# Optimization experiments

Hardware: AMD Instinct MI355X
Metric: run time of the kernel (lower is better)

Reference implementation:

```python
import jax, jax.numpy as jnp
import numpy as np

B, H, N, D = 4, 16, 2048, 128  # batch, num_head, maxlen, head_dim (qkdim == vdim)
EPS = 1e-6


def _act(x):
    # '1+elu' kernel feature map
    return jax.nn.elu(x) + 1.0


def _simple_rms_norm(x):
    # SimpleRMSNorm over the last dim: x / sqrt(mean(x^2) + eps), no learned scale
    ms = jnp.mean(jnp.square(x), axis=-1, keepdims=True)
    return x * jax.lax.rsqrt(ms + EPS)


def setup_inputs() -> dict:
    key = jax.random.key(0)
    kq, kk, kv, km = jax.random.split(key, 4)
    Q = jax.random.normal(kq, (B, H, N, D), dtype=jnp.float32)
    K = jax.random.normal(kk, (B, H, N, D), dtype=jnp.float32)
    V = jax.random.normal(kv, (B, H, N, D), dtype=jnp.float32)
    mask = jax.random.uniform(km, (B, N), dtype=jnp.float32)
    return {"Q": Q, "K": K, "V": V, "mask": mask}


def reference(Q, K, V, mask):
    m = mask[:, None, :, None]           # (B, 1, N, 1)
    Qf = _act(Q)                          # (B, H, N, D)
    Kf = _act(K) * m                      # masked feature-mapped keys
    Vf = V * m                            # masked values
    # non-causal linear attention: KV = sum_n K_n (x) V_n ; out = Q @ KV
    KV = jnp.einsum('bhnd,bhne->bhde', Kf, Vf)    # (B, H, D, D)
    out = jnp.einsum('bhde,bhnd->bhne', KV, Qf)   # (B, H, N, D)
    return _simple_rms_norm(out)
```

## Files before the change

### kernel.cpp

```cpp
#include <hip/hip_runtime.h>
#include <hip/hip_bf16.h>

#define NBH 64
#define NSEQ 2048
#define DD 128
#define EPS 1e-6f
#define NCH 16
#define CHROWS 128

typedef __bf16 bf16x8 __attribute__((ext_vector_type(8)));
typedef __bf16 bf16x4 __attribute__((ext_vector_type(4)));
typedef float  f32x4  __attribute__((ext_vector_type(4)));

__device__ __forceinline__ float elu1(float x) {
    return x > 0.f ? x + 1.f : __expf(x);
}

__global__ __launch_bounds__(256, 3) void kv_partial_kernel(
    const float* __restrict__ K, const float* __restrict__ V,
    const float* __restrict__ mask, __bf16* __restrict__ part)
{
    __shared__ __bf16 KfT[128 * 72];
    __shared__ __bf16 VfT[128 * 72];
    __shared__ float  mloc[CHROWS];

    const int s  = blockIdx.x;
    const int bh = blockIdx.y;
    const int b  = bh >> 4;
    const int t  = threadIdx.x;
    const int n0 = s * CHROWS;

    if (t < CHROWS) mloc[t] = mask[b * NSEQ + n0 + t];
    __syncthreads();

    const int rg   = t & 15;
    const int d0   = (t >> 4) * 8;
    const int lane = t & 63;
    const int w    = t >> 6;
    const int quad = lane >> 4;
    const int col  = lane & 15;

    f32x4 acc[2][8];
    #pragma unroll
    for (int i = 0; i < 2; ++i)
        #pragma unroll
        for (int dt = 0; dt < 8; ++dt) acc[i][dt] = (f32x4){0.f, 0.f, 0.f, 0.f};

    const float* Kb = K + ((size_t)bh * NSEQ + n0) * DD;
    const float* Vb = V + ((size_t)bh * NSEQ + n0) * DD;

    #pragma unroll
    for (int sub = 0; sub < 2; ++sub) {
        bf16x4 kc[8], vc[8];
        #pragma unroll
        for (int j = 0; j < 4; ++j) {
            const int nl = sub * 64 + rg * 4 + j;
            const float m = mloc[nl];
            f32x4 klo = *(const f32x4*)&Kb[(size_t)nl * DD + d0];
            f32x4 khi = *(const f32x4*)&Kb[(size_t)nl * DD + d0 + 4];
            f32x4 vlo = *(const f32x4*)&Vb[(size_t)nl * DD + d0];
            f32x4 vhi = *(const f32x4*)&Vb[(size_t)nl * DD + d0 + 4];
            #pragma unroll
            for (int c = 0; c < 4; ++c) {
                kc[c][j]     = (__bf16)(elu1(klo[c]) * m);
                kc[4 + c][j] = (__bf16)(elu1(khi[c]) * m);
                vc[c][j]     = (__bf16)(vlo[c] * m);
                vc[4 + c][j] = (__bf16)(vhi[c] * m);
            }
        }
        __syncthreads();
        #pragma unroll
        for (int c = 0; c < 8; ++c) {
            *(bf16x4*)&KfT[(d0 + c) * 72 + rg * 4] = kc[c];
            *(bf16x4*)&VfT[(d0 + c) * 72 + rg * 4] = vc[c];
        }
        __syncthreads();
        #pragma unroll
        for (int kk = 0; kk < 2; ++kk) {
            const int k0 = kk * 32 + quad * 8;
            bf16x8 a0 = *(bf16x8*)&VfT[((2 * w)     * 16 + col) * 72 + k0];
            bf16x8 a1 = *(bf16x8*)&VfT[((2 * w + 1) * 16 + col) * 72 + k0];
            #pragma unroll
            for (int dt = 0; dt < 8; ++dt) {
                bf16x8 bb = *(bf16x8*)&KfT[(dt * 16 + col) * 72 + k0];
                acc[0][dt] = __builtin_amdgcn_mfma_f32_16x16x32_bf16(a0, bb, acc[0][dt], 0, 0, 0);
                acc[1][dt] = __builtin_amdgcn_mfma_f32_16x16x32_bf16(a1, bb, acc[1][dt], 0, 0, 0);
            }
        }
    }

    __bf16* po = part + ((size_t)(bh * NCH + s) << 14);
    #pragma unroll
    for (int i = 0; i < 2; ++i) {
        #pragma unroll
        for (int r = 0; r < 4; ++r) {
            const int e = (2 * w + i) * 16 + quad * 4 + r;
            #pragma unroll
            for (int dt = 0; dt < 8; ++dt)
                po[e * 128 + dt * 16 + col] = (__bf16)acc[i][dt][r];
        }
    }
}

__global__ __launch_bounds__(256) void kv_reduce_kernel(
    const __bf16* __restrict__ part, __bf16* __restrict__ kvt)
{
    const int gid = blockIdx.x * 256 + threadIdx.x;
    const int i   = gid * 8;
    const int bh  = i >> 14;
    const int ii  = i & 16383;
    const __bf16* p = part + (((size_t)bh * NCH) << 14) + ii;
    float sum[8] = {0.f, 0.f, 0.f, 0.f, 0.f, 0.f, 0.f, 0.f};
    #pragma unroll
    for (int s = 0; s < NCH; ++s) {
        bf16x8 v = *(const bf16x8*)(p + ((size_t)s << 14));
        #pragma unroll
        for (int c = 0; c < 8; ++c) sum[c] += (float)v[c];
    }
    bf16x8 o;
    #pragma unroll
    for (int c = 0; c < 8; ++c) o[c] = (__bf16)sum[c];
    *(bf16x8*)&kvt[i] = o;
}

__global__ __launch_bounds__(256, 2) void qkv_norm_kernel(
    const float* __restrict__ Q, const __bf16* __restrict__ kvt,
    float* __restrict__ out)
{
    __shared__ __bf16 KVT[128 * 136];
    __shared__ __bf16 Qf[128 * 136];

    const int bh   = blockIdx.y;
    const int row0 = blockIdx.x * 128;
    const int t    = threadIdx.x;
    const int lane = t & 63;
    const int w    = t >> 6;
    const int quad = lane >> 4;
    const int col  = lane & 15;

    {
        const __bf16* src = kvt + ((size_t)bh << 14);
        #pragma unroll
        for (int i = 0; i < 8; ++i) {
            const int idx = i * 256 + t;
            const int e   = idx >> 4;
            const int dd  = (idx & 15) * 8;
            *(bf16x8*)&KVT[e * 136 + dd] = *(const bf16x8*)&src[e * 128 + dd];
        }
    }
    {
        const float* Qb = Q + ((size_t)bh * NSEQ + row0) * DD;
        const int qr  = t >> 1;
        const int qd0 = (t & 1) * 64;
        #pragma unroll
        for (int j = 0; j < 16; ++j) {
            f32x4 q = *(const f32x4*)&Qb[(size_t)qr * DD + qd0 + j * 4];
            bf16x4 qq;
            qq[0] = (__bf16)elu1(q[0]); qq[1] = (__bf16)elu1(q[1]);
            qq[2] = (__bf16)elu1(q[2]); qq[3] = (__bf16)elu1(q[3]);
            *(bf16x4*)&Qf[qr * 136 + qd0 + j * 4] = qq;
        }
    }
    __syncthreads();

    f32x4 acc[2][8];
    #pragma unroll
    for (int i = 0; i < 2; ++i)
        #pragma unroll
        for (int et = 0; et < 8; ++et) acc[i][et] = (f32x4){0.f, 0.f, 0.f, 0.f};

    #pragma unroll
    for (int kk = 0; kk < 4; ++kk) {
        const int k0 = kk * 32 + quad * 8;
        bf16x8 a0 = *(bf16x8*)&Qf[((2 * w)     * 16 + col) * 136 + k0];
        bf16x8 a1 = *(bf16x8*)&Qf[((2 * w + 1) * 16 + col) * 136 + k0];
        #pragma unroll
        for (int et = 0; et < 8; ++et) {
            bf16x8 bb = *(bf16x8*)&KVT[(et * 16 + col) * 136 + k0];
            acc[0][et] = __builtin_amdgcn_mfma_f32_16x16x32_bf16(a0, bb, acc[0][et], 0, 0, 0);
            acc[1][et] = __builtin_amdgcn_mfma_f32_16x16x32_bf16(a1, bb, acc[1][et], 0, 0, 0);
        }
    }

    float* ob = out + ((size_t)bh * NSEQ + row0) * DD;
    #pragma unroll
    for (int i = 0; i < 2; ++i) {
        #pragma unroll
        for (int r = 0; r < 4; ++r) {
            float p = 0.f;
            #pragma unroll
            for (int et = 0; et < 8; ++et) p += acc[i][et][r] * acc[i][et][r];
            p += __shfl_xor(p, 1);
            p += __shfl_xor(p, 2);
            p += __shfl_xor(p, 4);
            p += __shfl_xor(p, 8);
            const float scale = rsqrtf(p * (1.0f / 128.0f) + EPS);
            const int row = (2 * w + i) * 16 + quad * 4 + r;
            #pragma unroll
            for (int et = 0; et < 8; ++et)
                ob[row * DD + et * 16 + col] = acc[i][et][r] * scale;
        }
    }
}

extern "C" void kernel_launch(void* const* d_in, const int* in_sizes, int n_in,
                              void* d_out, int out_size, void* d_ws, size_t ws_size,
                              hipStream_t stream) {
    const float* Q    = (const float*)d_in[0];
    const float* K    = (const float*)d_in[1];
    const float* V    = (const float*)d_in[2];
    const float* mask = (const float*)d_in[3];
    float* out = (float*)d_out;

    __bf16* part = (__bf16*)d_ws;
    __bf16* kvt  = part + (size_t)NBH * NCH * 16384;

    kv_partial_kernel<<<dim3(NCH, NBH), 256, 0, stream>>>(K, V, mask, part);
    kv_reduce_kernel<<<512, 256, 0, stream>>>(part, kvt);
    qkv_norm_kernel<<<dim3(16, NBH), 256, 0, stream>>>(Q, kvt, out);
}
```

Before: 244.8 us.

## Stream K/V/Q via double-buffered global-to-LDS DMA and restructure KV layout

```diff
diff --git a/kernel.cpp b/kernel.cpp
--- a/kernel.cpp
+++ b/kernel.cpp
@@ -5,93 +5,112 @@
 #define NSEQ 2048
 #define DD 128
 #define EPS 1e-6f
-#define NCH 16
-#define CHROWS 128
+#define NCH 8
+#define G1 260
+#define G3 260
+#define KVG 264
+#define IMG_BYTES 33792
 
 typedef __bf16 bf16x8 __attribute__((ext_vector_type(8)));
-typedef __bf16 bf16x4 __attribute__((ext_vector_type(4)));
 typedef float  f32x4  __attribute__((ext_vector_type(4)));
 
 __device__ __forceinline__ float elu1(float x) {
     return x > 0.f ? x + 1.f : __expf(x);
 }
 
-__global__ __launch_bounds__(256, 3) void kv_partial_kernel(
+__device__ __forceinline__ void dma16(const void* g, void* l) {
+    __builtin_amdgcn_global_load_lds(
+        (const __attribute__((address_space(1))) unsigned int*)g,
+        (__attribute__((address_space(3))) unsigned int*)l, 16, 0, 0);
+}
+
+__global__ __launch_bounds__(256, 2) void kv_partial_kernel(
     const float* __restrict__ K, const float* __restrict__ V,
     const float* __restrict__ mask, __bf16* __restrict__ part)
 {
-    __shared__ __bf16 KfT[128 * 72];
-    __shared__ __bf16 VfT[128 * 72];
-    __shared__ float  mloc[CHROWS];
+    __shared__ __align__(16) float Kls[2][16 * G1];
+    __shared__ __align__(16) float Vls[2][16 * G1];
+    __shared__ float m2[256];
 
     const int s  = blockIdx.x;
     const int bh = blockIdx.y;
     const int b  = bh >> 4;
     const int t  = threadIdx.x;
-    const int n0 = s * CHROWS;
-
-    if (t < CHROWS) mloc[t] = mask[b * NSEQ + n0 + t];
-    __syncthreads();
-
-    const int rg   = t & 15;
-    const int d0   = (t >> 4) * 8;
+    const int n0 = s * 256;
+
+    { float m = mask[b * NSEQ + n0 + t]; m2[t] = m * m; }
+
     const int lane = t & 63;
     const int w    = t >> 6;
     const int quad = lane >> 4;
     const int col  = lane & 15;
 
-    f32x4 acc[2][8];
-    #pragma unroll
-    for (int i = 0; i < 2; ++i)
-        #pragma unroll
-        for (int dt = 0; dt < 8; ++dt) acc[i][dt] = (f32x4){0.f, 0.f, 0.f, 0.f};
-
     const float* Kb = K + ((size_t)bh * NSEQ + n0) * DD;
     const float* Vb = V + ((size_t)bh * NSEQ + n0) * DD;
 
-    #pragma unroll
-    for (int sub = 0; sub < 2; ++sub) {
-        bf16x4 kc[8], vc[8];
-        #pragma unroll
-        for (int j = 0; j < 4; ++j) {
-            const int nl = sub * 64 + rg * 4 + j;
-            const float m = mloc[nl];
-            f32x4 klo = *(const f32x4*)&Kb[(size_t)nl * DD + d0];
-            f32x4 khi = *(const f32x4*)&Kb[(size_t)nl * DD + d0 + 4];
-            f32x4 vlo = *(const f32x4*)&Vb[(size_t)nl * DD + d0];
-            f32x4 vhi = *(const f32x4*)&Vb[(size_t)nl * DD + d0 + 4];
-            #pragma unroll
-            for (int c = 0; c < 4; ++c) {
-                kc[c][j]     = (__bf16)(elu1(klo[c]) * m);
-                kc[4 + c][j] = (__bf16)(elu1(khi[c]) * m);
-                vc[c][j]     = (__bf16)(vlo[c] * m);
-                vc[4 + c][j] = (__bf16)(vhi[c] * m);
-            }
-        }
+    const int lrow = lane >> 5;
+    const int lc4  = (lane & 31) * 4;
+
+    f32x4 acc[2][8];
+    #pragma unroll
+    for (int i = 0; i < 2; ++i)
+        #pragma unroll
+        for (int dt = 0; dt < 8; ++dt) acc[i][dt] = (f32x4){0.f, 0.f, 0.f, 0.f};
+
+    #pragma unroll
+    for (int i = 0; i < 4; ++i) {
+        const int g   = w * 4 + i;
+        const int row = g * 2 + lrow;
+        dma16(Kb + (size_t)row * DD + lc4, &Kls[0][g * G1]);
+        dma16(Vb + (size_t)row * DD + lc4, &Vls[0][g * G1]);
+    }
+
+    for (int p = 0; p < 8; ++p) {
+        const int buf = p & 1;
         __syncthreads();
-        #pragma unroll
-        for (int c = 0; c < 8; ++c) {
-            *(bf16x4*)&KfT[(d0 + c) * 72 + rg * 4] = kc[c];
-            *(bf16x4*)&VfT[(d0 + c) * 72 + rg * 4] = vc[c];
-        }
-        __syncthreads();
-        #pragma unroll
-        for (int kk = 0; kk < 2; ++kk) {
-            const int k0 = kk * 32 + quad * 8;
-            bf16x8 a0 = *(bf16x8*)&VfT[((2 * w)     * 16 + col) * 72 + k0];
-            bf16x8 a1 = *(bf16x8*)&VfT[((2 * w + 1) * 16 + col) * 72 + k0];
-            #pragma unroll
-            for (int dt = 0; dt < 8; ++dt) {
-                bf16x8 bb = *(bf16x8*)&KfT[(dt * 16 + col) * 72 + k0];
-                acc[0][dt] = __builtin_amdgcn_mfma_f32_16x16x32_bf16(a0, bb, acc[0][dt], 0, 0, 0);
-                acc[1][dt] = __builtin_amdgcn_mfma_f32_16x16x32_bf16(a1, bb, acc[1][dt], 0, 0, 0);
-            }
+
+        if (p < 7) {
+            const int nb = (p + 1) & 1;
+            #pragma unroll
+            for (int i = 0; i < 4; ++i) {
+                const int g   = w * 4 + i;
+                const int row = (p + 1) * 32 + g * 2 + lrow;
+                dma16(Kb + (size_t)row * DD + lc4, &Kls[nb][g * G1]);
+                dma16(Vb + (size_t)row * DD + lc4, &Vls[nb][g * G1]);
+            }
+        }
+
+        bf16x8 a[2];
+        #pragma unroll
+        for (int i = 0; i < 2; ++i) {
+            const int e = (2 * w + i) * 16 + col;
+            #pragma unroll
+            for (int j = 0; j < 8; ++j) {
+                const int r = quad * 8 + j;
+                a[i][j] = (__bf16)Vls[buf][(r >> 1) * G1 + (r & 1) * 128 + e];
+            }
+        }
+        float mm[8];
+        #pragma unroll
+        for (int j = 0; j < 8; ++j) mm[j] = m2[p * 32 + quad * 8 + j];
+
+        #pragma unroll
+        for (int dt = 0; dt < 8; ++dt) {
+            bf16x8 bfrag;
+            #pragma unroll
+            for (int j = 0; j < 8; ++j) {
+                const int r = quad * 8 + j;
+                const float k = Kls[buf][(r >> 1) * G1 + (r & 1) * 128 + dt * 16 + col];
+                bfrag[j] = (__bf16)(elu1(k) * mm[j]);
+            }
+            acc[0][dt] = __builtin_amdgcn_mfma_f32_16x16x32_bf16(a[0], bfrag, acc[0][dt], 0, 0, 0);
+            acc[1][dt] = __builtin_amdgcn_mfma_f32_16x16x32_bf16(a[1], bfrag, acc[1][dt], 0, 0, 0);
         }
     }
 
     __bf16* po = part + ((size_t)(bh * NCH + s) << 14);
     #pragma unroll
-    for (int i = 0; i < 2; ++i) {
+    for (int i = 0; i < 2; ++i)
         #pragma unroll
         for (int r = 0; r < 4; ++r) {
             const int e = (2 * w + i) * 16 + quad * 4 + r;
@@ -99,17 +118,17 @@
             for (int dt = 0; dt < 8; ++dt)
                 po[e * 128 + dt * 16 + col] = (__bf16)acc[i][dt][r];
         }
-    }
 }
 
 __global__ __launch_bounds__(256) void kv_reduce_kernel(
-    const __bf16* __restrict__ part, __bf16* __restrict__ kvt)
+    const __bf16* __restrict__ part, __bf16* __restrict__ img)
 {
     const int gid = blockIdx.x * 256 + threadIdx.x;
-    const int i   = gid * 8;
-    const int bh  = i >> 14;
-    const int ii  = i & 16383;
-    const __bf16* p = part + (((size_t)bh * NCH) << 14) + ii;
+    const int d8  = gid & 15;
+    const int e   = (gid >> 4) & 127;
+    const int bh  = gid >> 11;
+
+    const __bf16* p = part + (((size_t)bh * NCH) << 14) + e * 128 + d8 * 8;
     float sum[8] = {0.f, 0.f, 0.f, 0.f, 0.f, 0.f, 0.f, 0.f};
     #pragma unroll
     for (int s = 0; s < NCH; ++s) {
@@ -120,85 +139,96 @@
     bf16x8 o;
     #pragma unroll
     for (int c = 0; c < 8; ++c) o[c] = (__bf16)sum[c];
-    *(bf16x8*)&kvt[i] = o;
-}
-
-__global__ __launch_bounds__(256, 2) void qkv_norm_kernel(
-    const float* __restrict__ Q, const __bf16* __restrict__ kvt,
+    __bf16* dst = img + (size_t)bh * (IMG_BYTES / 2)
+                + (e >> 1) * KVG + (e & 1) * 128 + d8 * 8;
+    *(bf16x8*)dst = o;
+}
+
+__global__ __launch_bounds__(128, 2) void qkv_norm_kernel(
+    const float* __restrict__ Q, const __bf16* __restrict__ img,
     float* __restrict__ out)
 {
-    __shared__ __bf16 KVT[128 * 136];
-    __shared__ __bf16 Qf[128 * 136];
+    __shared__ __align__(16) float  Qls[2][16 * G3];
+    __shared__ __align__(16) __bf16 KVls[64 * KVG];
 
     const int bh   = blockIdx.y;
-    const int row0 = blockIdx.x * 128;
+    const int row0 = blockIdx.x * 256;
     const int t    = threadIdx.x;
     const int lane = t & 63;
     const int w    = t >> 6;
     const int quad = lane >> 4;
     const int col  = lane & 15;
 
+    const float* Qb = Q + ((size_t)bh * NSEQ + row0) * DD;
+    const char*  ib = (const char*)img + (size_t)bh * IMG_BYTES;
+
+    const int lrow = lane >> 5;
+    const int lc4  = (lane & 31) * 4;
+
     {
-        const __bf16* src = kvt + ((size_t)bh << 14);
+        const int c0 = w ? 17 : 0;
+        const int c1 = w ? 33 : 17;
+        for (int c = c0; c < c1; ++c)
+            dma16(ib + c * 1024 + lane * 16, (char*)KVls + c * 1024);
         #pragma unroll
         for (int i = 0; i < 8; ++i) {
-            const int idx = i * 256 + t;
-            const int e   = idx >> 4;
-            const int dd  = (idx & 15) * 8;
-            *(bf16x8*)&KVT[e * 136 + dd] = *(const bf16x8*)&src[e * 128 + dd];
-        }
-    }
-    {
-        const float* Qb = Q + ((size_t)bh * NSEQ + row0) * DD;
-        const int qr  = t >> 1;
-        const int qd0 = (t & 1) * 64;
-        #pragma unroll
-        for (int j = 0; j < 16; ++j) {
-            f32x4 q = *(const f32x4*)&Qb[(size_t)qr * DD + qd0 + j * 4];
-            bf16x4 qq;
-            qq[0] = (__bf16)elu1(q[0]); qq[1] = (__bf16)elu1(q[1]);
-            qq[2] = (__bf16)elu1(q[2]); qq[3] = (__bf16)elu1(q[3]);
-            *(bf16x4*)&Qf[qr * 136 + qd0 + j * 4] = qq;
-        }
-    }
-    __syncthreads();
-
-    f32x4 acc[2][8];
-    #pragma unroll
-    for (int i = 0; i < 2; ++i)
-        #pragma unroll
-        for (int et = 0; et < 8; ++et) acc[i][et] = (f32x4){0.f, 0.f, 0.f, 0.f};
-
-    #pragma unroll
-    for (int kk = 0; kk < 4; ++kk) {
-        const int k0 = kk * 32 + quad * 8;
-        bf16x8 a0 = *(bf16x8*)&Qf[((2 * w)     * 16 + col) * 136 + k0];
-        bf16x8 a1 = *(bf16x8*)&Qf[((2 * w + 1) * 16 + col) * 136 + k0];
-        #pragma unroll
-        for (int et = 0; et < 8; ++et) {
-            bf16x8 bb = *(bf16x8*)&KVT[(et * 16 + col) * 136 + k0];
-            acc[0][et] = __builtin_amdgcn_mfma_f32_16x16x32_bf16(a0, bb, acc[0][et], 0, 0, 0);
-            acc[1][et] = __builtin_amdgcn_mfma_f32_16x16x32_bf16(a1, bb, acc[1][et], 0, 0, 0);
-        }
-    }
-
-    float* ob = out + ((size_t)bh * NSEQ + row0) * DD;
-    #pragma unroll
-    for (int i = 0; i < 2; ++i) {
+            const int g   = w * 8 + i;
+            const int row = g * 2 + lrow;
+            dma16(Qb + (size_t)row * DD + lc4, &Qls[0][g * G3]);
+        }
+    }
+
+    for (int p = 0; p < 8; ++p) {
+        const int buf = p & 1;
+        __syncthreads();
+
+        if (p < 7) {
+            const int nb = (p + 1) & 1;
+            #pragma unroll
+            for (int i = 0; i < 8; ++i) {
+                const int g   = w * 8 + i;
+                const int row = (p + 1) * 32 + g * 2 + lrow;
+                dma16(Qb + (size_t)row * DD + lc4, &Qls[nb][g * G3]);
+            }
+        }
+
+        f32x4 acc[8];
+        #pragma unroll
+        for (int et = 0; et < 8; ++et) acc[et] = (f32x4){0.f, 0.f, 0.f, 0.f};
+
+        const int rloc = w * 16 + col;
+        #pragma unroll
+        for (int kk = 0; kk < 4; ++kk) {
+            bf16x8 a;
+            #pragma unroll
+            for (int j = 0; j < 8; ++j) {
+                const int d = kk * 32 + quad * 8 + j;
+                a[j] = (__bf16)elu1(Qls[buf][(rloc >> 1) * G3 + (rloc & 1) * 128 + d]);
+            }
+            #pragma unroll
+            for (int et = 0; et < 8; ++et) {
+                const int e = et * 16 + col;
+                bf16x8 bb = *(const bf16x8*)&KVls[(e >> 1) * KVG + (e & 1) * 128
+                                                  + kk * 32 + quad * 8];
+                acc[et] = __builtin_amdgcn_mfma_f32_16x16x32_bf16(a, bb, acc[et], 0, 0, 0);
+            }
+        }
+
+        float* ob = out + ((size_t)bh * NSEQ + row0 + p * 32 + w * 16) * DD;
         #pragma unroll
         for (int r = 0; r < 4; ++r) {
-            float p = 0.f;
-            #pragma unroll
-            for (int et = 0; et < 8; ++et) p += acc[i][et][r] * acc[i][et][r];
-            p += __shfl_xor(p, 1);
-            p += __shfl_xor(p, 2);
-            p += __shfl_xor(p, 4);
-            p += __shfl_xor(p, 8);
-            const float scale = rsqrtf(p * (1.0f / 128.0f) + EPS);
-            const int row = (2 * w + i) * 16 + quad * 4 + r;
+            float ps = 0.f;
+            #pragma unroll
+            for (int et = 0; et < 8; ++et) ps += acc[et][r] * acc[et][r];
+            ps += __shfl_xor(ps, 1);
+            ps += __shfl_xor(ps, 2);
+            ps += __shfl_xor(ps, 4);
+            ps += __shfl_xor(ps, 8);
+            const float scale = rsqrtf(ps * (1.0f / 128.0f) + EPS);
+            const int row = quad * 4 + r;
             #pragma unroll
             for (int et = 0; et < 8; ++et)
-                ob[row * DD + et * 16 + col] = acc[i][et][r] * scale;
+                ob[row * DD + et * 16 + col] = acc[et][r] * scale;
         }
     }
 }
@@ -213,9 +243,9 @@
     float* out = (float*)d_out;
 
     __bf16* part = (__bf16*)d_ws;
-    __bf16* kvt  = part + (size_t)NBH * NCH * 16384;
+    __bf16* img  = (__bf16*)((char*)d_ws + (size_t)NBH * NCH * 16384 * 2);
 
     kv_partial_kernel<<<dim3(NCH, NBH), 256, 0, stream>>>(K, V, mask, part);
-    kv_reduce_kernel<<<512, 256, 0, stream>>>(part, kvt);
-    qkv_norm_kernel<<<dim3(16, NBH), 256, 0, stream>>>(Q, kvt, out);
-}
+    kv_reduce_kernel<<<512, 256, 0, stream>>>(part, img);
+    qkv_norm_kernel<<<dim3(8, NBH), 128, 0, stream>>>(Q, img, out);
+}
```

After: 242.6 us. Within noise of the previous version (-0.9%).
